# Performance work log

Hardware: AMD Instinct MI355X
Metric: run time of the kernel (lower is better)

Reference implementation:

```python
import jax, jax.numpy as jnp
import numpy as np

IN_F, OUT_F, USER_F = 1024, 512, 512
BSZ, S = 64, 256


def setup_inputs() -> dict:
    key = jax.random.key(0)
    k = jax.random.split(key, 7)
    X_doc = jax.random.normal(k[0], (BSZ, S, IN_F), dtype=jnp.float32)
    X_user = jax.random.normal(k[1], (BSZ, S, USER_F), dtype=jnp.float32)
    # xavier-normal-ish scaling for weights
    Wd = jax.random.normal(k[2], (OUT_F, IN_F), dtype=jnp.float32) * np.sqrt(2.0 / (IN_F + OUT_F))
    bd = jnp.zeros((OUT_F,), dtype=jnp.float32)
    Wu = jax.random.normal(k[3], (OUT_F, USER_F), dtype=jnp.float32) * np.sqrt(2.0 / (USER_F + OUT_F))
    bu = jnp.zeros((OUT_F,), dtype=jnp.float32)
    W = jax.random.normal(k[4], (OUT_F, OUT_F), dtype=jnp.float32) * np.sqrt(1.0 / OUT_F)
    return {"X_doc": X_doc, "X_user": X_user, "Wd": Wd, "bd": bd, "Wu": Wu, "bu": bu, "W": W}


def reference(X_doc, X_user, Wd, bd, Wu, bu, W):
    d = jnp.einsum('bsi,oi->bso', X_doc, Wd) + bd          # (b, s, out)
    u = jnp.einsum('bsi,oi->bso', X_user, Wu) + bu          # (b, s, out)
    d = d * jax.nn.sigmoid(u)
    u = u * jax.nn.sigmoid(d)
    att = jnp.tanh(jnp.einsum('bsd,de,bre->bsr', d, W, u))  # (b, s, s)
    score_d = jax.nn.softmax(att.mean(axis=2), axis=1)[..., None]  # (b, s, 1)
    score_u = jax.nn.softmax(att.mean(axis=1), axis=1)[..., None]  # (b, s, 1)
    attention_d = jnp.sum(score_d * d, axis=1)              # (b, out)
    attention_u = jnp.sum(score_u * u, axis=1)              # (b, out)
    return (attention_d, attention_u)
```

## Files before the change

kernel.cpp:

```cpp
#include <hip/hip_runtime.h>

#define S_ 256
#define BSZ_ 64
#define IN_F_ 1024
#define OUT_F_ 512
#define USER_F_ 512

typedef short short8 __attribute__((ext_vector_type(8)));
typedef float f32x4 __attribute__((ext_vector_type(4)));

__device__ __forceinline__ ushort f2bf(float f) {
  unsigned u = __float_as_uint(f);
  unsigned r = (u + 0x7FFFu + ((u >> 16) & 1u)) >> 16;
  return (ushort)r;
}
__device__ __forceinline__ float bf2f(unsigned hi16) {
  return __uint_as_float(hi16 << 16);
}
__device__ __forceinline__ float sigf(float x) {
  return 1.f / (1.f + __expf(-x));
}
__device__ __forceinline__ float tanh_safe(float x) {
  float ax = fabsf(x);
  float e = __expf(-2.f * ax);
  float r = (1.f - e) / (1.f + e);
  return copysignf(r, x);
}

__device__ __forceinline__ void gl_lds16(const ushort* g, ushort* l) {
  __builtin_amdgcn_global_load_lds(
      (const __attribute__((address_space(1))) void*)g,
      (__attribute__((address_space(3))) void*)l, 16, 0, 0);
}

__global__ void convert_bf16(const float* __restrict__ in, ushort* __restrict__ out, long n) {
  long i = ((long)blockIdx.x * blockDim.x + threadIdx.x) * 4;
  if (i + 3 < n) {
    float4 v = *(const float4*)(in + i);
    ushort4 o;
    o.x = f2bf(v.x); o.y = f2bf(v.y); o.z = f2bf(v.z); o.w = f2bf(v.w);
    *(ushort4*)(out + i) = o;
  }
}

__global__ void convert_transpose_w(const float* __restrict__ in, ushort* __restrict__ out) {
  int i = blockIdx.x * blockDim.x + threadIdx.x;
  int e = i >> 9, d = i & 511;
  out[i] = f2bf(in[d * 512 + e]);
}

__global__ void zerof(float* __restrict__ p, int n) {
  int i = blockIdx.x * 256 + threadIdx.x;
  if (i < n) p[i] = 0.f;
}

template <int ROWS>
__device__ __forceinline__ void stage_tile(const ushort* __restrict__ g, int K,
                                           ushort* lds, int w, int lane) {
  const int rin = lane >> 3;
  const int c = lane & 7;
#pragma unroll
  for (int i = 0; i < ROWS / 32; ++i) {
    int r = w * (ROWS / 4) + i * 8 + rin;
    int gc = c ^ (r & 7);
    gl_lds16(g + (long)r * K + gc * 8, lds + w * (ROWS / 4) * 64 + i * 512);
  }
}

__device__ __forceinline__ short8 frag(const ushort* lds, int row, int kk, int q) {
  int pc = (kk * 4 + q) ^ (row & 7);
  return *(const short8*)(lds + row * 64 + pc * 8);
}

__device__ __forceinline__ void compute_step(const ushort* As, const ushort* Bs,
                                             f32x4 acc[2][4], int wr, int wc,
                                             int mlane, int q) {
#pragma unroll
  for (int kk = 0; kk < 2; ++kk) {
    short8 af[2], bfr[4];
#pragma unroll
    for (int r = 0; r < 2; ++r) af[r] = frag(As, wr * 32 + r * 16 + mlane, kk, q);
#pragma unroll
    for (int c = 0; c < 4; ++c) bfr[c] = frag(Bs, wc * 64 + c * 16 + mlane, kk, q);
#pragma unroll
    for (int r = 0; r < 2; ++r)
#pragma unroll
      for (int c = 0; c < 4; ++c)
        acc[r][c] = __builtin_amdgcn_mfma_f32_16x16x32_bf16(af[r], bfr[c], acc[r][c], 0, 0, 0);
  }
}

template <int NSTEP>
__device__ __forceinline__ void gemm_loop(const ushort* __restrict__ A,
                                          const ushort* __restrict__ B, int K,
                                          ushort* As, ushort* Bs, f32x4 acc[2][4],
                                          int w, int lane, int wr, int wc,
                                          int mlane, int q) {
#pragma unroll 1
  for (int k = 0; k < NSTEP; ++k) {
    stage_tile<64>(A + k * 64, K, As, w, lane);
    stage_tile<128>(B + k * 64, K, Bs, w, lane);
    __syncthreads();
    compute_step(As, Bs, acc, wr, wc, mlane, q);
    __syncthreads();
  }
}

#define ACC_ZERO(a)                             \
  _Pragma("unroll") for (int r = 0; r < 2; ++r) \
  _Pragma("unroll") for (int c = 0; c < 4; ++c) { \
    a[r][c][0] = 0.f; a[r][c][1] = 0.f; a[r][c][2] = 0.f; a[r][c][3] = 0.f; }

__global__ __launch_bounds__(256, 4) void gemm_du(
    const ushort* __restrict__ Xd, const ushort* __restrict__ Wd,
    const float* __restrict__ bd,
    const ushort* __restrict__ Xu, const ushort* __restrict__ Wu,
    const float* __restrict__ bu,
    ushort* __restrict__ dg, ushort* __restrict__ ug) {
  __shared__ ushort sm[12288];
  ushort* As = sm; ushort* Bs = sm + 4096;
  const int i = blockIdx.x;
  const int k8 = i & 7, j = i >> 3;
  const int by = k8 * 32 + (j >> 2), bx = j & 3;
  const int tid = threadIdx.x, lane = tid & 63, w = tid >> 6;
  const int wr = w >> 1, wc = w & 1, mlane = lane & 15, q = lane >> 4;
  const int m0 = by * 64, n0 = bx * 128;

  f32x4 accd[2][4]; ACC_ZERO(accd);
  gemm_loop<16>(Xd + (long)m0 * 1024, Wd + (long)n0 * 1024, 1024,
                As, Bs, accd, w, lane, wr, wc, mlane, q);
  f32x4 accu[2][4]; ACC_ZERO(accu);
  gemm_loop<8>(Xu + (long)m0 * 512, Wu + (long)n0 * 512, 512,
               As, Bs, accu, w, lane, wr, wc, mlane, q);

#pragma unroll
  for (int c = 0; c < 4; ++c) {
    const int gn = n0 + wc * 64 + c * 16 + mlane;
    const float bdv = bd[gn], buv = bu[gn];
#pragma unroll
    for (int r = 0; r < 2; ++r)
#pragma unroll
      for (int ii = 0; ii < 4; ++ii) {
        const int gm = m0 + wr * 32 + r * 16 + q * 4 + ii;
        const long idx = (long)gm * OUT_F_ + gn;
        float dp = accd[r][c][ii] + bdv;
        float up = accu[r][c][ii] + buv;
        float dgv = dp * sigf(up);
        float ugv = up * sigf(dgv);
        dg[idx] = f2bf(dgv);
        ug[idx] = f2bf(ugv);
      }
  }
}

__global__ __launch_bounds__(256, 4) void gemm_t(
    const ushort* __restrict__ dgp, const ushort* __restrict__ Wt,
    ushort* __restrict__ tout) {
  __shared__ ushort sm[12288];
  ushort* As = sm; ushort* Bs = sm + 4096;
  const int i = blockIdx.x;
  const int k8 = i & 7, j = i >> 3;
  const int by = k8 * 32 + (j >> 2), bx = j & 3;
  const int tid = threadIdx.x, lane = tid & 63, w = tid >> 6;
  const int wr = w >> 1, wc = w & 1, mlane = lane & 15, q = lane >> 4;
  const int m0 = by * 64, n0 = bx * 128;

  f32x4 acc[2][4]; ACC_ZERO(acc);
  gemm_loop<8>(dgp + (long)m0 * 512, Wt + (long)n0 * 512, 512,
               As, Bs, acc, w, lane, wr, wc, mlane, q);

#pragma unroll
  for (int c = 0; c < 4; ++c) {
    const int gn = n0 + wc * 64 + c * 16 + mlane;
#pragma unroll
    for (int r = 0; r < 2; ++r)
#pragma unroll
      for (int ii = 0; ii < 4; ++ii) {
        const int gm = m0 + wr * 32 + r * 16 + q * 4 + ii;
        tout[(long)gm * OUT_F_ + gn] = f2bf(acc[r][c][ii]);
      }
  }
}

__global__ __launch_bounds__(256, 4) void gemm_att(
    const ushort* __restrict__ t, const ushort* __restrict__ ug,
    float* __restrict__ rowlog, float* __restrict__ collog) {
  __shared__ ushort sm[12288];
  ushort* As = sm; ushort* Bs = sm + 4096;
  const int i = blockIdx.x;
  const int k8 = i & 7, j = i >> 3;
  const int b = k8 * 8 + (j >> 3);
  const int l = j & 7, by = l >> 1, bx = l & 1;
  const int tid = threadIdx.x, lane = tid & 63, w = tid >> 6;
  const int wr = w >> 1, wc = w & 1, mlane = lane & 15, q = lane >> 4;
  const ushort* A = t + (long)b * (S_ * OUT_F_) + (long)by * 64 * 512;
  const ushort* B = ug + (long)b * (S_ * OUT_F_) + (long)bx * 128 * 512;

  f32x4 acc[2][4]; ACC_ZERO(acc);
  gemm_loop<8>(A, B, 512, As, Bs, acc, w, lane, wr, wc, mlane, q);

  float rs[2][4], cs[4];
#pragma unroll
  for (int r = 0; r < 2; ++r)
#pragma unroll
    for (int ii = 0; ii < 4; ++ii) rs[r][ii] = 0.f;
#pragma unroll
  for (int c = 0; c < 4; ++c) cs[c] = 0.f;
#pragma unroll
  for (int r = 0; r < 2; ++r)
#pragma unroll
    for (int c = 0; c < 4; ++c)
#pragma unroll
      for (int ii = 0; ii < 4; ++ii) {
        float v = tanh_safe(acc[r][c][ii]);
        rs[r][ii] += v;
        cs[c] += v;
      }
#pragma unroll
  for (int m = 1; m < 16; m <<= 1)
#pragma unroll
    for (int r = 0; r < 2; ++r)
#pragma unroll
      for (int ii = 0; ii < 4; ++ii) rs[r][ii] += __shfl_xor(rs[r][ii], m, 64);
#pragma unroll
  for (int m = 16; m < 64; m <<= 1)
#pragma unroll
    for (int c = 0; c < 4; ++c) cs[c] += __shfl_xor(cs[c], m, 64);

  float* rsum = (float*)sm;
  float* csum = ((float*)sm) + 64;
  if (tid < 64) rsum[tid] = 0.f;
  else if (tid < 192) csum[tid - 64] = 0.f;
  __syncthreads();
  if (mlane == 0) {
#pragma unroll
    for (int r = 0; r < 2; ++r)
#pragma unroll
      for (int ii = 0; ii < 4; ++ii)
        atomicAdd(&rsum[wr * 32 + r * 16 + q * 4 + ii], rs[r][ii]);
  }
  if (q == 0) {
#pragma unroll
    for (int c = 0; c < 4; ++c) atomicAdd(&csum[wc * 64 + c * 16 + mlane], cs[c]);
  }
  __syncthreads();
  if (tid < 64)
    atomicAdd(&rowlog[b * S_ + by * 64 + tid], rsum[tid]);
  else if (tid < 192)
    atomicAdd(&collog[b * S_ + bx * 128 + (tid - 64)], csum[tid - 64]);
}

__device__ __forceinline__ float block_max(float v, float* buf, int tid) {
  buf[tid] = v; __syncthreads();
  for (int s = 128; s > 0; s >>= 1) {
    if (tid < s) buf[tid] = fmaxf(buf[tid], buf[tid + s]);
    __syncthreads();
  }
  float r = buf[0]; __syncthreads();
  return r;
}
__device__ __forceinline__ float block_sum(float v, float* buf, int tid) {
  buf[tid] = v; __syncthreads();
  for (int s = 128; s > 0; s >>= 1) {
    if (tid < s) buf[tid] = buf[tid] + buf[tid + s];
    __syncthreads();
  }
  float r = buf[0]; __syncthreads();
  return r;
}

__global__ __launch_bounds__(256) void finalize(
    const float* __restrict__ rowlog, const float* __restrict__ collog,
    const ushort* __restrict__ dg, const ushort* __restrict__ ug,
    float* __restrict__ out) {
  __shared__ float sd[S_], su[S_], buf[S_];
  const int b = blockIdx.x, tid = threadIdx.x;

  const float rowmean = rowlog[b * S_ + tid] * (1.f / (float)S_);
  const float colmean = collog[b * S_ + tid] * (1.f / (float)S_);

  float md = block_max(rowmean, buf, tid);
  float ed = __expf(rowmean - md);
  float sds = block_sum(ed, buf, tid);
  sd[tid] = ed / sds;
  float mu = block_max(colmean, buf, tid);
  float eu = __expf(colmean - mu);
  float sus = block_sum(eu, buf, tid);
  su[tid] = eu / sus;
  __syncthreads();

  const ushort* dgb = dg + (long)b * (S_ * OUT_F_);
  const ushort* ugb = ug + (long)b * (S_ * OUT_F_);
  float ad0 = 0.f, ad1 = 0.f, au0 = 0.f, au1 = 0.f;
  const int o = 2 * tid;
  for (int s = 0; s < S_; ++s) {
    const float wd = sd[s], wu = su[s];
    unsigned dv = *(const unsigned*)(dgb + s * OUT_F_ + o);
    unsigned uv = *(const unsigned*)(ugb + s * OUT_F_ + o);
    ad0 += wd * bf2f(dv & 0xffffu); ad1 += wd * bf2f(dv >> 16);
    au0 += wu * bf2f(uv & 0xffffu); au1 += wu * bf2f(uv >> 16);
  }
  out[b * OUT_F_ + o] = ad0;
  out[b * OUT_F_ + o + 1] = ad1;
  out[BSZ_ * OUT_F_ + b * OUT_F_ + o] = au0;
  out[BSZ_ * OUT_F_ + b * OUT_F_ + o + 1] = au1;
}

extern "C" void kernel_launch(void* const* d_in, const int* in_sizes, int n_in,
                              void* d_out, int out_size, void* d_ws, size_t ws_size,
                              hipStream_t stream) {
  (void)in_sizes; (void)n_in; (void)out_size; (void)ws_size;
  const float* Xd = (const float*)d_in[0];
  const float* Xu = (const float*)d_in[1];
  const float* Wd = (const float*)d_in[2];
  const float* bd = (const float*)d_in[3];
  const float* Wu = (const float*)d_in[4];
  const float* bu = (const float*)d_in[5];
  const float* W  = (const float*)d_in[6];
  float* out = (float*)d_out;
  char* ws = (char*)d_ws;

  ushort* Xd_bf  = (ushort*)(ws + 0L);
  ushort* Xu_bf  = (ushort*)(ws + 33554432L);
  ushort* Wd_bf  = (ushort*)(ws + 50331648L);
  ushort* Wu_bf  = (ushort*)(ws + 51380224L);
  ushort* Wt_bf  = (ushort*)(ws + 51904512L);
  ushort* dg     = (ushort*)(ws + 52428800L);
  ushort* ug     = (ushort*)(ws + 69206016L);
  ushort* t_bf   = (ushort*)(ws + 85983232L);
  float*  rowlog = (float*)(ws + 102760448L);
  float*  collog = (float*)(ws + 102825984L);

  convert_bf16<<<16384, 256, 0, stream>>>(Xd, Xd_bf, 16777216L);
  convert_bf16<<<8192, 256, 0, stream>>>(Xu, Xu_bf, 8388608L);
  convert_bf16<<<512, 256, 0, stream>>>(Wd, Wd_bf, 524288L);
  convert_bf16<<<256, 256, 0, stream>>>(Wu, Wu_bf, 262144L);
  convert_transpose_w<<<1024, 256, 0, stream>>>(W, Wt_bf);
  zerof<<<128, 256, 0, stream>>>(rowlog, 32768);

  dim3 blk(256);
  gemm_du<<<1024, blk, 0, stream>>>(Xd_bf, Wd_bf, bd, Xu_bf, Wu_bf, bu, dg, ug);
  gemm_t<<<1024, blk, 0, stream>>>(dg, Wt_bf, t_bf);
  gemm_att<<<512, blk, 0, stream>>>(t_bf, ug, rowlog, collog);
  finalize<<<64, 256, 0, stream>>>(rowlog, collog, dg, ug, out);
}
```

Before: 223.6 us.

## Fuse fp32-to-bf16 conversion of activations into GEMM A-tile staging

Removes the separate conversion passes over X_doc and X_user. The GEMM now loads fp32 activations directly and packs them to bf16 into swizzled LDS with register stores. The small weight conversions, the W transpose and the rowlog zeroing are merged into a single prep launch. This avoids writing and re-reading about 48MB of bf16 copies plus several launches. In exchange, the A tile moves through registers synchronously instead of using async global-to-LDS loads, and the fp32 reads double the A-side bytes per GEMM.

```diff
diff --git a/kernel.cpp b/kernel.cpp
--- a/kernel.cpp
+++ b/kernel.cpp
@@ -1,4 +1,5 @@
 #include <hip/hip_runtime.h>
+#include <hip/hip_bf16.h>
 
 #define S_ 256
 #define BSZ_ 64
@@ -17,6 +18,11 @@
 __device__ __forceinline__ float bf2f(unsigned hi16) {
   return __uint_as_float(hi16 << 16);
 }
+__device__ __forceinline__ unsigned pkbf(float a, float b) {
+  union { __hip_bfloat162 h; unsigned u; } x;
+  x.h = __float22bfloat162_rn(float2{a, b});
+  return x.u;
+}
 __device__ __forceinline__ float sigf(float x) {
   return 1.f / (1.f + __expf(-x));
 }
@@ -33,25 +39,27 @@
       (__attribute__((address_space(3))) void*)l, 16, 0, 0);
 }
 
-__global__ void convert_bf16(const float* __restrict__ in, ushort* __restrict__ out, long n) {
-  long i = ((long)blockIdx.x * blockDim.x + threadIdx.x) * 4;
-  if (i + 3 < n) {
-    float4 v = *(const float4*)(in + i);
-    ushort4 o;
-    o.x = f2bf(v.x); o.y = f2bf(v.y); o.z = f2bf(v.z); o.w = f2bf(v.w);
-    *(ushort4*)(out + i) = o;
-  }
-}
-
-__global__ void convert_transpose_w(const float* __restrict__ in, ushort* __restrict__ out) {
-  int i = blockIdx.x * blockDim.x + threadIdx.x;
-  int e = i >> 9, d = i & 511;
-  out[i] = f2bf(in[d * 512 + e]);
-}
-
-__global__ void zerof(float* __restrict__ p, int n) {
+__global__ void prep(const float* __restrict__ Wd, const float* __restrict__ Wu,
+                     const float* __restrict__ W, float* __restrict__ rowlog,
+                     ushort* __restrict__ Wd_bf, ushort* __restrict__ Wu_bf,
+                     ushort* __restrict__ Wt_bf) {
   int i = blockIdx.x * 256 + threadIdx.x;
-  if (i < n) p[i] = 0.f;
+  if (i < 131072) {
+    float4 v = ((const float4*)Wd)[i];
+    ushort4 o; o.x = f2bf(v.x); o.y = f2bf(v.y); o.z = f2bf(v.z); o.w = f2bf(v.w);
+    ((ushort4*)Wd_bf)[i] = o;
+  } else if (i < 196608) {
+    int j = i - 131072;
+    float4 v = ((const float4*)Wu)[j];
+    ushort4 o; o.x = f2bf(v.x); o.y = f2bf(v.y); o.z = f2bf(v.z); o.w = f2bf(v.w);
+    ((ushort4*)Wu_bf)[j] = o;
+  } else if (i < 458752) {
+    int j = i - 196608;
+    Wt_bf[j] = f2bf(W[(j & 511) * 512 + (j >> 9)]);
+  } else {
+    int j = i - 458752;
+    ((float4*)rowlog)[j] = float4{0.f, 0.f, 0.f, 0.f};
+  }
 }
 
 template <int ROWS>
@@ -65,6 +73,21 @@
     int gc = c ^ (r & 7);
     gl_lds16(g + (long)r * K + gc * 8, lds + w * (ROWS / 4) * 64 + i * 512);
   }
+}
+
+__device__ __forceinline__ void stage_a_f32(const float* __restrict__ g, int K,
+                                            ushort* As, int t) {
+  const int row = t >> 2, seg = t & 3;
+  const float4* p = (const float4*)(g + (long)row * K + seg * 16);
+  float4 v0 = p[0], v1 = p[1], v2 = p[2], v3 = p[3];
+  uint4 w0, w1;
+  w0.x = pkbf(v0.x, v0.y); w0.y = pkbf(v0.z, v0.w);
+  w0.z = pkbf(v1.x, v1.y); w0.w = pkbf(v1.z, v1.w);
+  w1.x = pkbf(v2.x, v2.y); w1.y = pkbf(v2.z, v2.w);
+  w1.z = pkbf(v3.x, v3.y); w1.w = pkbf(v3.z, v3.w);
+  ushort* base = As + row * 64;
+  *(uint4*)(base + ((seg * 2) ^ (row & 7)) * 8) = w0;
+  *(uint4*)(base + ((seg * 2 + 1) ^ (row & 7)) * 8) = w1;
 }
 
 __device__ __forceinline__ short8 frag(const ushort* lds, int row, int kk, int q) {
@@ -106,15 +129,32 @@
   }
 }
 
+template <int NSTEP>
+__device__ __forceinline__ void gemm_loop_f32a(const float* __restrict__ Af,
+                                               const ushort* __restrict__ B, int K,
+                                               ushort* As, ushort* Bs,
+                                               f32x4 acc[2][4], int t, int w,
+                                               int lane, int wr, int wc,
+                                               int mlane, int q) {
+#pragma unroll 1
+  for (int k = 0; k < NSTEP; ++k) {
+    stage_a_f32(Af + k * 64, K, As, t);
+    stage_tile<128>(B + k * 64, K, Bs, w, lane);
+    __syncthreads();
+    compute_step(As, Bs, acc, wr, wc, mlane, q);
+    __syncthreads();
+  }
+}
+
 #define ACC_ZERO(a)                             \
   _Pragma("unroll") for (int r = 0; r < 2; ++r) \
   _Pragma("unroll") for (int c = 0; c < 4; ++c) { \
     a[r][c][0] = 0.f; a[r][c][1] = 0.f; a[r][c][2] = 0.f; a[r][c][3] = 0.f; }
 
 __global__ __launch_bounds__(256, 4) void gemm_du(
-    const ushort* __restrict__ Xd, const ushort* __restrict__ Wd,
+    const float* __restrict__ Xd, const ushort* __restrict__ Wd,
     const float* __restrict__ bd,
-    const ushort* __restrict__ Xu, const ushort* __restrict__ Wu,
+    const float* __restrict__ Xu, const ushort* __restrict__ Wu,
     const float* __restrict__ bu,
     ushort* __restrict__ dg, ushort* __restrict__ ug) {
   __shared__ ushort sm[12288];
@@ -127,11 +167,11 @@
   const int m0 = by * 64, n0 = bx * 128;
 
   f32x4 accd[2][4]; ACC_ZERO(accd);
-  gemm_loop<16>(Xd + (long)m0 * 1024, Wd + (long)n0 * 1024, 1024,
-                As, Bs, accd, w, lane, wr, wc, mlane, q);
+  gemm_loop_f32a<16>(Xd + (long)m0 * 1024, Wd + (long)n0 * 1024, 1024,
+                     As, Bs, accd, tid, w, lane, wr, wc, mlane, q);
   f32x4 accu[2][4]; ACC_ZERO(accu);
-  gemm_loop<8>(Xu + (long)m0 * 512, Wu + (long)n0 * 512, 512,
-               As, Bs, accu, w, lane, wr, wc, mlane, q);
+  gemm_loop_f32a<8>(Xu + (long)m0 * 512, Wu + (long)n0 * 512, 512,
+                    As, Bs, accu, tid, w, lane, wr, wc, mlane, q);
 
 #pragma unroll
   for (int c = 0; c < 4; ++c) {
@@ -320,26 +360,19 @@
   float* out = (float*)d_out;
   char* ws = (char*)d_ws;
 
-  ushort* Xd_bf  = (ushort*)(ws + 0L);
-  ushort* Xu_bf  = (ushort*)(ws + 33554432L);
-  ushort* Wd_bf  = (ushort*)(ws + 50331648L);
-  ushort* Wu_bf  = (ushort*)(ws + 51380224L);
-  ushort* Wt_bf  = (ushort*)(ws + 51904512L);
-  ushort* dg     = (ushort*)(ws + 52428800L);
-  ushort* ug     = (ushort*)(ws + 69206016L);
-  ushort* t_bf   = (ushort*)(ws + 85983232L);
-  float*  rowlog = (float*)(ws + 102760448L);
-  float*  collog = (float*)(ws + 102825984L);
-
-  convert_bf16<<<16384, 256, 0, stream>>>(Xd, Xd_bf, 16777216L);
-  convert_bf16<<<8192, 256, 0, stream>>>(Xu, Xu_bf, 8388608L);
-  convert_bf16<<<512, 256, 0, stream>>>(Wd, Wd_bf, 524288L);
-  convert_bf16<<<256, 256, 0, stream>>>(Wu, Wu_bf, 262144L);
-  convert_transpose_w<<<1024, 256, 0, stream>>>(W, Wt_bf);
-  zerof<<<128, 256, 0, stream>>>(rowlog, 32768);
+  ushort* Wd_bf  = (ushort*)(ws + 0L);
+  ushort* Wu_bf  = (ushort*)(ws + 1048576L);
+  ushort* Wt_bf  = (ushort*)(ws + 1572864L);
+  ushort* dg     = (ushort*)(ws + 2097152L);
+  ushort* ug     = (ushort*)(ws + 18874368L);
+  ushort* t_bf   = (ushort*)(ws + 35651584L);
+  float*  rowlog = (float*)(ws + 52428800L);
+  float*  collog = (float*)(ws + 52494336L);
+
+  prep<<<1824, 256, 0, stream>>>(Wd, Wu, W, rowlog, Wd_bf, Wu_bf, Wt_bf);
 
   dim3 blk(256);
-  gemm_du<<<1024, blk, 0, stream>>>(Xd_bf, Wd_bf, bd, Xu_bf, Wu_bf, bu, dg, ug);
+  gemm_du<<<1024, blk, 0, stream>>>(Xd, Wd_bf, bd, Xu, Wu_bf, bu, dg, ug);
   gemm_t<<<1024, blk, 0, stream>>>(dg, Wt_bf, t_bf);
   gemm_att<<<512, blk, 0, stream>>>(t_bf, ug, rowlog, collog);
   finalize<<<64, 256, 0, stream>>>(rowlog, collog, dg, ug, out);
```

Result: no change. 225.4 us (+0.8%).

## Fuse t-projection and attention GEMMs keeping t tile in LDS; merge prep kernels

Applied to the files above, without the earlier changes.

Combines the d·W and t·uᵀ GEMMs into one kernel where each block computes a 32-row slice of t into shared memory, then multiplies it against all of u for that batch, writing row sums directly and column sums atomically. This removes the global round trip of the intermediate t tensor and a launch. The separate conversion and zeroing kernels are merged into one prep launch, and finalize is split across four blocks per batch for more parallelism. The fused kernel uses 64 KB LDS and lower occupancy with unpipelined staging, which may limit GEMM throughput.

```diff
diff --git a/kernel.cpp b/kernel.cpp
--- a/kernel.cpp
+++ b/kernel.cpp
@@ -1,4 +1,5 @@
 #include <hip/hip_runtime.h>
+#include <hip/hip_bf16.h>
 
 #define S_ 256
 #define BSZ_ 64
@@ -33,25 +34,39 @@
       (__attribute__((address_space(3))) void*)l, 16, 0, 0);
 }
 
-__global__ void convert_bf16(const float* __restrict__ in, ushort* __restrict__ out, long n) {
-  long i = ((long)blockIdx.x * blockDim.x + threadIdx.x) * 4;
-  if (i + 3 < n) {
-    float4 v = *(const float4*)(in + i);
-    ushort4 o;
-    o.x = f2bf(v.x); o.y = f2bf(v.y); o.z = f2bf(v.z); o.w = f2bf(v.w);
-    *(ushort4*)(out + i) = o;
-  }
-}
-
-__global__ void convert_transpose_w(const float* __restrict__ in, ushort* __restrict__ out) {
-  int i = blockIdx.x * blockDim.x + threadIdx.x;
-  int e = i >> 9, d = i & 511;
-  out[i] = f2bf(in[d * 512 + e]);
-}
-
-__global__ void zerof(float* __restrict__ p, int n) {
+__global__ void prep(const float* __restrict__ Xd, const float* __restrict__ Xu,
+                     const float* __restrict__ Wd, const float* __restrict__ Wu,
+                     const float* __restrict__ W,
+                     ushort* __restrict__ Xd_bf, ushort* __restrict__ Xu_bf,
+                     ushort* __restrict__ Wd_bf, ushort* __restrict__ Wu_bf,
+                     ushort* __restrict__ Wt_bf, float* __restrict__ rowlog) {
   int i = blockIdx.x * 256 + threadIdx.x;
-  if (i < n) p[i] = 0.f;
+  if (i < 4194304) {
+    float4 v = ((const float4*)Xd)[i];
+    ushort4 o; o.x = f2bf(v.x); o.y = f2bf(v.y); o.z = f2bf(v.z); o.w = f2bf(v.w);
+    ((ushort4*)Xd_bf)[i] = o;
+  } else if (i < 6291456) {
+    int j = i - 4194304;
+    float4 v = ((const float4*)Xu)[j];
+    ushort4 o; o.x = f2bf(v.x); o.y = f2bf(v.y); o.z = f2bf(v.z); o.w = f2bf(v.w);
+    ((ushort4*)Xu_bf)[j] = o;
+  } else if (i < 6422528) {
+    int j = i - 6291456;
+    float4 v = ((const float4*)Wd)[j];
+    ushort4 o; o.x = f2bf(v.x); o.y = f2bf(v.y); o.z = f2bf(v.z); o.w = f2bf(v.w);
+    ((ushort4*)Wd_bf)[j] = o;
+  } else if (i < 6488064) {
+    int j = i - 6422528;
+    float4 v = ((const float4*)Wu)[j];
+    ushort4 o; o.x = f2bf(v.x); o.y = f2bf(v.y); o.z = f2bf(v.z); o.w = f2bf(v.w);
+    ((ushort4*)Wu_bf)[j] = o;
+  } else if (i < 6750208) {
+    int j = i - 6488064;
+    Wt_bf[j] = f2bf(W[(j & 511) * 512 + (j >> 9)]);
+  } else {
+    int j = i - 6750208;
+    ((float4*)rowlog)[j] = float4{0.f, 0.f, 0.f, 0.f};
+  }
 }
 
 template <int ROWS>
@@ -66,10 +81,22 @@
     gl_lds16(g + (long)r * K + gc * 8, lds + w * (ROWS / 4) * 64 + i * 512);
   }
 }
+__device__ __forceinline__ void stage_tile32(const ushort* __restrict__ g, int K,
+                                             ushort* lds, int w, int lane) {
+  const int rin = lane >> 3, c = lane & 7;
+  int r = w * 8 + rin;
+  int gc = c ^ (r & 7);
+  gl_lds16(g + (long)r * K + gc * 8, lds + w * 512);
+}
 
 __device__ __forceinline__ short8 frag(const ushort* lds, int row, int kk, int q) {
   int pc = (kk * 4 + q) ^ (row & 7);
   return *(const short8*)(lds + row * 64 + pc * 8);
+}
+__device__ __forceinline__ short8 frag512(const ushort* lds, int row, int k,
+                                          int kk, int q) {
+  int pc = (kk * 4 + q) ^ (row & 7);
+  return *(const short8*)(lds + row * 512 + k * 64 + pc * 8);
 }
 
 __device__ __forceinline__ void compute_step(const ushort* As, const ushort* Bs,
@@ -153,57 +180,94 @@
   }
 }
 
-__global__ __launch_bounds__(256, 4) void gemm_t(
-    const ushort* __restrict__ dgp, const ushort* __restrict__ Wt,
-    ushort* __restrict__ tout) {
-  __shared__ ushort sm[12288];
-  ushort* As = sm; ushort* Bs = sm + 4096;
+__global__ __launch_bounds__(256, 2) void gemm_tatt(
+    const ushort* __restrict__ dg, const ushort* __restrict__ Wt,
+    const ushort* __restrict__ ug, float* __restrict__ rowlog,
+    float* __restrict__ collog) {
+  __shared__ ushort sm[32768];
+  ushort* t_lds = sm;
+  ushort* AsT = sm + 16384;
+  ushort* BsT = sm + 18432;
+  ushort* BsU = sm + 16384;
   const int i = blockIdx.x;
-  const int k8 = i & 7, j = i >> 3;
-  const int by = k8 * 32 + (j >> 2), bx = j & 3;
+  const int xcd = i & 7, j = i >> 3;
+  const int b = xcd * 8 + (j >> 3);
+  const int by = j & 7;
   const int tid = threadIdx.x, lane = tid & 63, w = tid >> 6;
-  const int wr = w >> 1, wc = w & 1, mlane = lane & 15, q = lane >> 4;
-  const int m0 = by * 64, n0 = bx * 128;
+  const int mlane = lane & 15, q = lane >> 4;
+  const ushort* dgs = dg + (long)b * (S_ * OUT_F_) + (long)by * 32 * 512;
+  const ushort* ugb = ug + (long)b * (S_ * OUT_F_);
+
+#pragma unroll 1
+  for (int nc = 0; nc < 4; ++nc) {
+    f32x4 acc[2][2];
+#pragma unroll
+    for (int r = 0; r < 2; ++r)
+#pragma unroll
+      for (int c = 0; c < 2; ++c) {
+        acc[r][c][0] = 0.f; acc[r][c][1] = 0.f; acc[r][c][2] = 0.f; acc[r][c][3] = 0.f;
+      }
+    const ushort* Bw = Wt + (long)(nc * 128) * 512;
+#pragma unroll 1
+    for (int k = 0; k < 8; ++k) {
+      stage_tile32(dgs + k * 64, 512, AsT, w, lane);
+      stage_tile<128>(Bw + k * 64, 512, BsT, w, lane);
+      __syncthreads();
+#pragma unroll
+      for (int kk = 0; kk < 2; ++kk) {
+        short8 af[2], bfr[2];
+#pragma unroll
+        for (int r = 0; r < 2; ++r) af[r] = frag(AsT, r * 16 + mlane, kk, q);
+#pragma unroll
+        for (int c = 0; c < 2; ++c)
+          bfr[c] = frag(BsT, w * 32 + c * 16 + mlane, kk, q);
+#pragma unroll
+        for (int r = 0; r < 2; ++r)
+#pragma unroll
+          for (int c = 0; c < 2; ++c)
+            acc[r][c] = __builtin_amdgcn_mfma_f32_16x16x32_bf16(af[r], bfr[c], acc[r][c], 0, 0, 0);
+      }
+      __syncthreads();
+    }
+#pragma unroll
+    for (int r = 0; r < 2; ++r)
+#pragma unroll
+      for (int c = 0; c < 2; ++c)
+#pragma unroll
+        for (int ii = 0; ii < 4; ++ii) {
+          int rr = r * 16 + q * 4 + ii;
+          int col = nc * 128 + w * 32 + c * 16 + mlane;
+          int cc = col >> 3;
+          int ph = (cc & ~7) | ((cc & 7) ^ (rr & 7));
+          t_lds[rr * 512 + ph * 8 + (col & 7)] = f2bf(acc[r][c][ii]);
+        }
+  }
 
   f32x4 acc[2][4]; ACC_ZERO(acc);
-  gemm_loop<8>(dgp + (long)m0 * 512, Wt + (long)n0 * 512, 512,
-               As, Bs, acc, w, lane, wr, wc, mlane, q);
-
-#pragma unroll
-  for (int c = 0; c < 4; ++c) {
-    const int gn = n0 + wc * 64 + c * 16 + mlane;
-#pragma unroll
-    for (int r = 0; r < 2; ++r)
-#pragma unroll
-      for (int ii = 0; ii < 4; ++ii) {
-        const int gm = m0 + wr * 32 + r * 16 + q * 4 + ii;
-        tout[(long)gm * OUT_F_ + gn] = f2bf(acc[r][c][ii]);
-      }
-  }
-}
-
-__global__ __launch_bounds__(256, 4) void gemm_att(
-    const ushort* __restrict__ t, const ushort* __restrict__ ug,
-    float* __restrict__ rowlog, float* __restrict__ collog) {
-  __shared__ ushort sm[12288];
-  ushort* As = sm; ushort* Bs = sm + 4096;
-  const int i = blockIdx.x;
-  const int k8 = i & 7, j = i >> 3;
-  const int b = k8 * 8 + (j >> 3);
-  const int l = j & 7, by = l >> 1, bx = l & 1;
-  const int tid = threadIdx.x, lane = tid & 63, w = tid >> 6;
-  const int wr = w >> 1, wc = w & 1, mlane = lane & 15, q = lane >> 4;
-  const ushort* A = t + (long)b * (S_ * OUT_F_) + (long)by * 64 * 512;
-  const ushort* B = ug + (long)b * (S_ * OUT_F_) + (long)bx * 128 * 512;
-
-  f32x4 acc[2][4]; ACC_ZERO(acc);
-  gemm_loop<8>(A, B, 512, As, Bs, acc, w, lane, wr, wc, mlane, q);
-
-  float rs[2][4], cs[4];
-#pragma unroll
-  for (int r = 0; r < 2; ++r)
-#pragma unroll
-    for (int ii = 0; ii < 4; ++ii) rs[r][ii] = 0.f;
+#pragma unroll 1
+  for (int k = 0; k < 8; ++k) {
+    stage_tile<256>(ugb + k * 64, 512, BsU, w, lane);
+    __syncthreads();
+#pragma unroll
+    for (int kk = 0; kk < 2; ++kk) {
+      short8 af[2], bfr[4];
+#pragma unroll
+      for (int r = 0; r < 2; ++r) af[r] = frag512(t_lds, r * 16 + mlane, k, kk, q);
+#pragma unroll
+      for (int c = 0; c < 4; ++c)
+        bfr[c] = frag(BsU, w * 64 + c * 16 + mlane, kk, q);
+#pragma unroll
+      for (int r = 0; r < 2; ++r)
+#pragma unroll
+        for (int c = 0; c < 4; ++c)
+          acc[r][c] = __builtin_amdgcn_mfma_f32_16x16x32_bf16(af[r], bfr[c], acc[r][c], 0, 0, 0);
+    }
+    __syncthreads();
+  }
+
+  float rs[8], cs[4];
+#pragma unroll
+  for (int x = 0; x < 8; ++x) rs[x] = 0.f;
 #pragma unroll
   for (int c = 0; c < 4; ++c) cs[c] = 0.f;
 #pragma unroll
@@ -213,41 +277,33 @@
 #pragma unroll
       for (int ii = 0; ii < 4; ++ii) {
         float v = tanh_safe(acc[r][c][ii]);
-        rs[r][ii] += v;
+        rs[r * 4 + ii] += v;
         cs[c] += v;
       }
 #pragma unroll
   for (int m = 1; m < 16; m <<= 1)
 #pragma unroll
-    for (int r = 0; r < 2; ++r)
-#pragma unroll
-      for (int ii = 0; ii < 4; ++ii) rs[r][ii] += __shfl_xor(rs[r][ii], m, 64);
+    for (int x = 0; x < 8; ++x) rs[x] += __shfl_xor(rs[x], m, 64);
 #pragma unroll
   for (int m = 16; m < 64; m <<= 1)
 #pragma unroll
     for (int c = 0; c < 4; ++c) cs[c] += __shfl_xor(cs[c], m, 64);
 
-  float* rsum = (float*)sm;
-  float* csum = ((float*)sm) + 64;
-  if (tid < 64) rsum[tid] = 0.f;
-  else if (tid < 192) csum[tid - 64] = 0.f;
+  float* rsum = (float*)BsU;
+  if (tid < 32) rsum[tid] = 0.f;
   __syncthreads();
   if (mlane == 0) {
 #pragma unroll
-    for (int r = 0; r < 2; ++r)
-#pragma unroll
-      for (int ii = 0; ii < 4; ++ii)
-        atomicAdd(&rsum[wr * 32 + r * 16 + q * 4 + ii], rs[r][ii]);
+    for (int x = 0; x < 8; ++x)
+      atomicAdd(&rsum[(x >> 2) * 16 + q * 4 + (x & 3)], rs[x]);
   }
   if (q == 0) {
 #pragma unroll
-    for (int c = 0; c < 4; ++c) atomicAdd(&csum[wc * 64 + c * 16 + mlane], cs[c]);
+    for (int c = 0; c < 4; ++c)
+      atomicAdd(&collog[b * S_ + w * 64 + c * 16 + mlane], cs[c]);
   }
   __syncthreads();
-  if (tid < 64)
-    atomicAdd(&rowlog[b * S_ + by * 64 + tid], rsum[tid]);
-  else if (tid < 192)
-    atomicAdd(&collog[b * S_ + bx * 128 + (tid - 64)], csum[tid - 64]);
+  if (tid < 32) rowlog[b * S_ + by * 32 + tid] = rsum[tid];
 }
 
 __device__ __forceinline__ float block_max(float v, float* buf, int tid) {
@@ -274,7 +330,8 @@
     const ushort* __restrict__ dg, const ushort* __restrict__ ug,
     float* __restrict__ out) {
   __shared__ float sd[S_], su[S_], buf[S_];
-  const int b = blockIdx.x, tid = threadIdx.x;
+  const int b = blockIdx.x >> 2, oc = blockIdx.x & 3;
+  const int tid = threadIdx.x;
 
   const float rowmean = rowlog[b * S_ + tid] * (1.f / (float)S_);
   const float colmean = collog[b * S_ + tid] * (1.f / (float)S_);
@@ -289,21 +346,13 @@
   su[tid] = eu / sus;
   __syncthreads();
 
-  const ushort* dgb = dg + (long)b * (S_ * OUT_F_);
-  const ushort* ugb = ug + (long)b * (S_ * OUT_F_);
-  float ad0 = 0.f, ad1 = 0.f, au0 = 0.f, au1 = 0.f;
-  const int o = 2 * tid;
-  for (int s = 0; s < S_; ++s) {
-    const float wd = sd[s], wu = su[s];
-    unsigned dv = *(const unsigned*)(dgb + s * OUT_F_ + o);
-    unsigned uv = *(const unsigned*)(ugb + s * OUT_F_ + o);
-    ad0 += wd * bf2f(dv & 0xffffu); ad1 += wd * bf2f(dv >> 16);
-    au0 += wu * bf2f(uv & 0xffffu); au1 += wu * bf2f(uv >> 16);
-  }
-  out[b * OUT_F_ + o] = ad0;
-  out[b * OUT_F_ + o + 1] = ad1;
-  out[BSZ_ * OUT_F_ + b * OUT_F_ + o] = au0;
-  out[BSZ_ * OUT_F_ + b * OUT_F_ + o + 1] = au1;
+  const int o = oc * 128 + (tid & 127);
+  const ushort* src = (tid < 128) ? dg : ug;
+  const float* sw = (tid < 128) ? sd : su;
+  const ushort* p = src + (long)b * (S_ * OUT_F_) + o;
+  float a = 0.f;
+  for (int s = 0; s < S_; ++s) a += sw[s] * bf2f((unsigned)p[s * OUT_F_]);
+  out[((tid < 128) ? 0 : BSZ_ * OUT_F_) + b * OUT_F_ + o] = a;
 }
 
 extern "C" void kernel_launch(void* const* d_in, const int* in_sizes, int n_in,
@@ -327,20 +376,14 @@
   ushort* Wt_bf  = (ushort*)(ws + 51904512L);
   ushort* dg     = (ushort*)(ws + 52428800L);
   ushort* ug     = (ushort*)(ws + 69206016L);
-  ushort* t_bf   = (ushort*)(ws + 85983232L);
-  float*  rowlog = (float*)(ws + 102760448L);
-  float*  collog = (float*)(ws + 102825984L);
-
-  convert_bf16<<<16384, 256, 0, stream>>>(Xd, Xd_bf, 16777216L);
-  convert_bf16<<<8192, 256, 0, stream>>>(Xu, Xu_bf, 8388608L);
-  convert_bf16<<<512, 256, 0, stream>>>(Wd, Wd_bf, 524288L);
-  convert_bf16<<<256, 256, 0, stream>>>(Wu, Wu_bf, 262144L);
-  convert_transpose_w<<<1024, 256, 0, stream>>>(W, Wt_bf);
-  zerof<<<128, 256, 0, stream>>>(rowlog, 32768);
+  float*  rowlog = (float*)(ws + 85983232L);
+  float*  collog = (float*)(ws + 86048768L);
+
+  prep<<<26400, 256, 0, stream>>>(Xd, Xu, Wd, Wu, W, Xd_bf, Xu_bf,
+                                  Wd_bf, Wu_bf, Wt_bf, rowlog);
 
   dim3 blk(256);
   gemm_du<<<1024, blk, 0, stream>>>(Xd_bf, Wd_bf, bd, Xu_bf, Wu_bf, bu, dg, ug);
-  gemm_t<<<1024, blk, 0, stream>>>(dg, Wt_bf, t_bf);
-  gemm_att<<<512, blk, 0, stream>>>(t_bf, ug, rowlog, collog);
-  finalize<<<64, 256, 0, stream>>>(rowlog, collog, dg, ug, out);
-}
+  gemm_tatt<<<512, blk, 0, stream>>>(dg, Wt_bf, ug, rowlog, collog);
+  finalize<<<256, 256, 0, stream>>>(rowlog, collog, dg, ug, out);
+}
```

Result: no change. 222.2 us (-0.6%).
